# Kernel tuning notes

Measured on AMD Instinct MI355X. Metric: run time of the kernel, lower is better.

Reference implementation:

```python
import jax, jax.numpy as jnp
import numpy as np

EMBED_DIM = 2048
HEAD_DIM = 128
BLOCK = 2048
BATCH = 8


def setup_inputs() -> dict:
    key = jax.random.key(0)
    kx, kq, kk, kv = jax.random.split(key, 4)
    x = jax.random.normal(kx, (BATCH, BLOCK, EMBED_DIM), dtype=jnp.float32)
    # torch nn.Linear(embed_dim, head_dim, bias=False) weight shape: [head_dim, embed_dim]
    s = 1.0 / np.sqrt(EMBED_DIM)
    Wq = jax.random.uniform(kq, (HEAD_DIM, EMBED_DIM), jnp.float32, -s, s)
    Wk = jax.random.uniform(kk, (HEAD_DIM, EMBED_DIM), jnp.float32, -s, s)
    Wv = jax.random.uniform(kv, (HEAD_DIM, EMBED_DIM), jnp.float32, -s, s)
    return {"x": x, "Wq": Wq, "Wk": Wk, "Wv": Wv}


def reference(x, Wq, Wk, Wv):
    B, T, C = x.shape
    # projections: y = x @ W.T
    q = jnp.einsum('btc,hc->bth', x, Wq)   # [B,T,H]
    k = jnp.einsum('btc,hc->bth', x, Wk)
    v = jnp.einsum('btc,hc->bth', x, Wv)
    # NOTE: original scales by embed_dim**0.5, not head_dim**0.5
    scale = 1.0 / jnp.sqrt(jnp.float32(C))
    logits = jnp.einsum('bth,bsh->bts', q, k) * scale  # [B,T,T]
    # causal mask (is_decoder=True)
    causal = jnp.tril(jnp.ones((T, T), dtype=bool))
    logits = jnp.where(causal, logits, -jnp.inf)
    weights = jax.nn.softmax(logits, axis=-1)
    attention = jnp.einsum('bts,bsh->bth', weights, v)  # [B,T,H]
    return attention
```

## Files before the change

### kernel.cpp

```cpp
#include <hip/hip_runtime.h>
#include <hip/hip_bf16.h>
#include <stdint.h>

constexpr int B    = 8;
constexpr int T    = 2048;
constexpr int EMB  = 2048;
constexpr int HD   = 128;
constexpr int M    = B * T;
constexpr int NW   = 3 * HD;

typedef __attribute__((ext_vector_type(8))) short short8;
typedef __attribute__((ext_vector_type(4))) float f32x4;

__device__ inline unsigned short f2bf(float f) {
    union { float f; unsigned int u; } v; v.f = f;
    unsigned int x = v.u;
    unsigned int r = (x + 0x7FFFu + ((x >> 16) & 1u)) >> 16;
    return (unsigned short)r;
}

__device__ inline unsigned int cvt_pk_bf16(float a, float b) {
    unsigned int r;
    asm volatile("v_cvt_pk_bf16_f32 %0, %1, %2" : "=v"(r) : "v"(a), "v"(b));
    return r;
}

__global__ __launch_bounds__(256) void conv_w(
    const float* __restrict__ Wq, const float* __restrict__ Wk, const float* __restrict__ Wv,
    unsigned short* __restrict__ Wb)
{
    int base = (blockIdx.x * 256 + threadIdx.x) * 8;
    int row = base >> 11, col = base & 2047;
    const float* src;
    if (row < 128)      src = Wq + (size_t)row * EMB + col;
    else if (row < 256) src = Wk + (size_t)(row - 128) * EMB + col;
    else                src = Wv + (size_t)(row - 256) * EMB + col;
    float4 a = *(const float4*)src;
    float4 b = *(const float4*)(src + 4);
    short8 sv;
    sv[0] = f2bf(a.x); sv[1] = f2bf(a.y); sv[2] = f2bf(a.z); sv[3] = f2bf(a.w);
    sv[4] = f2bf(b.x); sv[5] = f2bf(b.y); sv[6] = f2bf(b.z); sv[7] = f2bf(b.w);
    *(short8*)(Wb + base) = sv;
}

constexpr int PBM = 32;
constexpr int PBK = 64;
constexpr int PNT = EMB / PBK;

__global__ __launch_bounds__(256) void qkv_proj(
    const float* __restrict__ x, const unsigned short* __restrict__ Wb,
    unsigned short* __restrict__ Qb, unsigned short* __restrict__ Kb,
    unsigned short* __restrict__ VtG)
{
    __shared__ unsigned short Asm[2][PBM * PBK];
    __shared__ unsigned short Bsm[NW * PBK];

    const int m0   = blockIdx.x * PBM;
    const int tid  = threadIdx.x;
    const int lane = tid & 63;
    const int w    = tid >> 6;
    const int lo   = lane & 15;
    const int hi   = lane >> 4;

    const int ar = tid >> 3;
    const int as = tid & 7;
    const float* asrc = x + (size_t)(m0 + ar) * EMB + as * 8;

    f32x4 acc[2][6];
#pragma unroll
    for (int i = 0; i < 2; ++i)
#pragma unroll
        for (int j = 0; j < 6; ++j) acc[i][j] = (f32x4)0.0f;

    float4 a0, a1;
    auto issueA = [&](int k0) {
        a0 = *(const float4*)(asrc + k0);
        a1 = *(const float4*)(asrc + k0 + 4);
    };
    auto writeA = [&](int buf) {
        uint4 p;
        p.x = cvt_pk_bf16(a0.x, a0.y);
        p.y = cvt_pk_bf16(a0.z, a0.w);
        p.z = cvt_pk_bf16(a1.x, a1.y);
        p.w = cvt_pk_bf16(a1.z, a1.w);
        int ps = as ^ (ar & 7);
        *(uint4*)&Asm[buf][ar * PBK + ps * 8] = p;
    };
    auto stageB = [&](int k0) {
#pragma unroll
        for (int it = 0; it < 12; ++it) {
            int c = it * 256 + tid;
            int row = c >> 3;
            int lseg = (c & 7) ^ (row & 7);
            __builtin_amdgcn_global_load_lds(
                (const __attribute__((address_space(1))) unsigned int*)
                    (Wb + (size_t)row * EMB + k0 + lseg * 8),
                (__attribute__((address_space(3))) unsigned int*)
                    ((char*)&Bsm[0] + (it * 256 + w * 64) * 16),
                16, 0, 0);
        }
    };
    auto compute = [&](int buf) {
#pragma unroll
        for (int kk = 0; kk < 2; ++kk) {
            short8 af[2], bf[6];
#pragma unroll
            for (int i = 0; i < 2; ++i) {
                int R = i * 16 + lo;
                int pseg = (kk * 4 + hi) ^ (R & 7);
                af[i] = *(const short8*)&Asm[buf][R * PBK + pseg * 8];
            }
#pragma unroll
            for (int j = 0; j < 6; ++j) {
                int n = w * 96 + j * 16 + lo;
                int pseg = (kk * 4 + hi) ^ (n & 7);
                bf[j] = *(const short8*)&Bsm[n * PBK + pseg * 8];
            }
#pragma unroll
            for (int i = 0; i < 2; ++i)
#pragma unroll
                for (int j = 0; j < 6; ++j)
                    acc[i][j] = __builtin_amdgcn_mfma_f32_16x16x32_bf16(af[i], bf[j], acc[i][j], 0, 0, 0);
        }
    };

    issueA(0);
    stageB(0);
    writeA(0);
    asm volatile("s_waitcnt vmcnt(0) lgkmcnt(0)" ::: "memory");
    __builtin_amdgcn_s_barrier();

    int cur = 0;
    for (int t = 0; t < PNT; ++t) {
        if (t + 1 < PNT) issueA((t + 1) * PBK);
        compute(cur);
        __builtin_amdgcn_s_barrier();
        if (t + 1 < PNT) {
            stageB((t + 1) * PBK);
            writeA(cur ^ 1);
            asm volatile("s_waitcnt vmcnt(0) lgkmcnt(0)" ::: "memory");
            __builtin_amdgcn_s_barrier();
        }
        cur ^= 1;
    }

    const int b = m0 >> 11;
#pragma unroll
    for (int i = 0; i < 2; ++i) {
        int mrow0 = m0 + i * 16 + hi * 4;
#pragma unroll
        for (int j = 0; j < 6; ++j) {
            int cw = w * 6 + j;
            int colbase = cw * 16 + lo;
            if (cw < 8) {
#pragma unroll
                for (int r = 0; r < 4; ++r)
                    Qb[(size_t)(mrow0 + r) * HD + colbase] = f2bf(acc[i][j][r]);
            } else if (cw < 16) {
#pragma unroll
                for (int r = 0; r < 4; ++r)
                    Kb[(size_t)(mrow0 + r) * HD + (colbase - 128)] = f2bf(acc[i][j][r]);
            } else {
                int h = colbase - 256;
                int tloc = mrow0 - b * T;
                ushort4 pv;
                pv.x = f2bf(acc[i][j][0]); pv.y = f2bf(acc[i][j][1]);
                pv.z = f2bf(acc[i][j][2]); pv.w = f2bf(acc[i][j][3]);
                *(ushort4*)(VtG + ((size_t)(b * HD + h)) * T + tloc) = pv;
            }
        }
    }
}

constexpr int QB = 64;
constexpr int KB = 64;
constexpr int STILES = 8;

__global__ __launch_bounds__(256) void attn_fwd(
    const unsigned short* __restrict__ Qb,
    const unsigned short* __restrict__ Kb,
    const unsigned short* __restrict__ VtG,
    float* __restrict__ out,
    float* __restrict__ part_o, float* __restrict__ part_ml,
    int use_split)
{
    const int b  = blockIdx.y;
    int bx = blockIdx.x;
    int qt, s, nsplit;
    if (use_split) {
        if (bx < 8)       { qt = bx;               s = 0; }
        else if (bx < 24) { qt = 8  + (bx - 8) / 2;  s = (bx - 8) & 1; }
        else if (bx < 48) { qt = 16 + (bx - 24) / 3; s = (bx - 24) % 3; }
        else              { qt = 24 + (bx - 48) / 4; s = (bx - 48) & 3; }
        nsplit = qt / 8 + 1;
    } else {
        qt = bx; s = 0; nsplit = 1;
    }
    const int q0 = qt * QB;
    int t0 = s * STILES;
    int t1 = t0 + STILES; if (t1 > qt + 1) t1 = qt + 1;

    const int tid  = threadIdx.x;
    const int lane = tid & 63;
    const int w    = tid >> 6;
    const int lo   = lane & 15;
    const int hi   = lane >> 4;

    __shared__ unsigned short Ks[KB][HD + 8];
    __shared__ unsigned short Vt[HD][KB + 16];
    __shared__ unsigned short Ps[QB][KB + 8];

    short8 qf[4];
    {
        int row = q0 + w * 16 + lo;
        const unsigned short* qp = Qb + ((size_t)b * T + row) * HD + hi * 8;
#pragma unroll
        for (int ks = 0; ks < 4; ++ks) qf[ks] = *(const short8*)(qp + ks * 32);
    }

    float mrow[4], lrow[4];
    f32x4 o[8];
#pragma unroll
    for (int r = 0; r < 4; ++r) { mrow[r] = -1e30f; lrow[r] = 0.0f; }
#pragma unroll
    for (int n = 0; n < 8; ++n) o[n] = (f32x4)0.0f;

    const float scale2 = 0.022097086912079608f * 1.4426950408889634f;
    const int qrow_base = q0 + w * 16 + hi * 4;

    for (int t = t0; t < t1; ++t) {
        const int kv0 = t * KB;
#pragma unroll
        for (int it = 0; it < 4; ++it) {
            int c = tid + it * 256;
            int row = c >> 4, c8 = (c & 15) * 8;
            *(short8*)&Ks[row][c8] =
                *(const short8*)(Kb + ((size_t)b * T + kv0 + row) * HD + c8);
        }
#pragma unroll
        for (int it = 0; it < 4; ++it) {
            int c = tid + it * 256;
            int row = c >> 3, c8 = (c & 7) * 8;
            *(short8*)&Vt[row][c8] =
                *(const short8*)(VtG + (size_t)(b * HD + row) * T + kv0 + c8);
        }
        __syncthreads();

        f32x4 sa[4];
#pragma unroll
        for (int j = 0; j < 4; ++j) sa[j] = (f32x4)0.0f;
#pragma unroll
        for (int ks = 0; ks < 4; ++ks) {
#pragma unroll
            for (int j = 0; j < 4; ++j) {
                short8 bf = *(const short8*)&Ks[j * 16 + lo][ks * 32 + hi * 8];
                sa[j] = __builtin_amdgcn_mfma_f32_16x16x32_bf16(qf[ks], bf, sa[j], 0, 0, 0);
            }
        }

        const bool diag = (t == qt);
        float alpha[4];
#pragma unroll
        for (int r = 0; r < 4; ++r) {
            const int qrow = qrow_base + r;
            float rm = -1e30f;
#pragma unroll
            for (int j = 0; j < 4; ++j) {
                float v = sa[j][r] * scale2;
                if (diag) {
                    int kv = kv0 + j * 16 + lo;
                    v = (kv <= qrow) ? v : -1e30f;
                }
                sa[j][r] = v;
                rm = fmaxf(rm, v);
            }
            rm = fmaxf(rm, __shfl_xor(rm, 1));
            rm = fmaxf(rm, __shfl_xor(rm, 2));
            rm = fmaxf(rm, __shfl_xor(rm, 4));
            rm = fmaxf(rm, __shfl_xor(rm, 8));
            float mn = fmaxf(mrow[r], rm);
            alpha[r] = exp2f(mrow[r] - mn);
            mrow[r] = mn;
            float ls = 0.0f;
#pragma unroll
            for (int j = 0; j < 4; ++j) {
                float p = exp2f(sa[j][r] - mn);
                sa[j][r] = p;
                ls += p;
            }
            ls += __shfl_xor(ls, 1);
            ls += __shfl_xor(ls, 2);
            ls += __shfl_xor(ls, 4);
            ls += __shfl_xor(ls, 8);
            lrow[r] = lrow[r] * alpha[r] + ls;
        }
#pragma unroll
        for (int n = 0; n < 8; ++n)
#pragma unroll
            for (int r = 0; r < 4; ++r) o[n][r] *= alpha[r];

#pragma unroll
        for (int r = 0; r < 4; ++r)
#pragma unroll
            for (int j = 0; j < 4; ++j)
                Ps[w * 16 + hi * 4 + r][j * 16 + lo] = f2bf(sa[j][r]);
        __syncthreads();

#pragma unroll
        for (int ks = 0; ks < 2; ++ks) {
            short8 af = *(const short8*)&Ps[w * 16 + lo][ks * 32 + hi * 8];
#pragma unroll
            for (int n = 0; n < 8; ++n) {
                short8 bv = *(const short8*)&Vt[n * 16 + lo][ks * 32 + hi * 8];
                o[n] = __builtin_amdgcn_mfma_f32_16x16x32_bf16(af, bv, o[n], 0, 0, 0);
            }
        }
        __syncthreads();
    }

    if (nsplit == 1) {
#pragma unroll
        for (int n = 0; n < 8; ++n) {
            int h = n * 16 + lo;
#pragma unroll
            for (int r = 0; r < 4; ++r) {
                int row = qrow_base + r;
                out[((size_t)b * T + row) * HD + h] = o[n][r] / lrow[r];
            }
        }
    } else {
        const size_t slot = (size_t)(b * 32 + qt) * 4 + s;
        float* po = part_o + slot * (QB * HD);
#pragma unroll
        for (int n = 0; n < 8; ++n) {
            int h = n * 16 + lo;
#pragma unroll
            for (int r = 0; r < 4; ++r)
                po[(w * 16 + hi * 4 + r) * HD + h] = o[n][r];
        }
        if (lo == 0) {
            float* pm = part_ml + slot * (QB * 2);
#pragma unroll
            for (int r = 0; r < 4; ++r) {
                pm[(w * 16 + hi * 4 + r) * 2 + 0] = mrow[r];
                pm[(w * 16 + hi * 4 + r) * 2 + 1] = lrow[r];
            }
        }
    }
}

__global__ __launch_bounds__(256) void attn_combine(
    const float* __restrict__ part_o, const float* __restrict__ part_ml,
    float* __restrict__ out)
{
    const int qt = 8 + blockIdx.x;
    const int b  = blockIdx.y;
    const int ns = qt / 8 + 1;
    const int tid = threadIdx.x;
    const int row = tid >> 2;
    const int c0  = (tid & 3) * 32;
    const size_t slot0 = (size_t)(b * 32 + qt) * 4;

    float mi[4], li[4];
    float m = -1e30f;
#pragma unroll 4
    for (int i = 0; i < ns; ++i) {
        mi[i] = part_ml[(slot0 + i) * (QB * 2) + row * 2 + 0];
        li[i] = part_ml[(slot0 + i) * (QB * 2) + row * 2 + 1];
        m = fmaxf(m, mi[i]);
    }
    float L = 0.0f, f[4];
#pragma unroll 4
    for (int i = 0; i < ns; ++i) {
        f[i] = exp2f(mi[i] - m);
        L += li[i] * f[i];
    }
    const float inv = 1.0f / L;

    float4 acc[8];
#pragma unroll
    for (int k = 0; k < 8; ++k) acc[k] = make_float4(0.f, 0.f, 0.f, 0.f);
#pragma unroll 4
    for (int i = 0; i < ns; ++i) {
        const float4* src = (const float4*)(part_o + (slot0 + i) * (QB * HD) + row * HD + c0);
#pragma unroll
        for (int k = 0; k < 8; ++k) {
            float4 v = src[k];
            acc[k].x += f[i] * v.x; acc[k].y += f[i] * v.y;
            acc[k].z += f[i] * v.z; acc[k].w += f[i] * v.w;
        }
    }
    float4* dst = (float4*)(out + ((size_t)b * T + qt * QB + row) * HD + c0);
#pragma unroll
    for (int k = 0; k < 8; ++k) {
        float4 v = acc[k];
        dst[k] = make_float4(v.x * inv, v.y * inv, v.z * inv, v.w * inv);
    }
}

extern "C" void kernel_launch(void* const* d_in, const int* in_sizes, int n_in,
                              void* d_out, int out_size, void* d_ws, size_t ws_size,
                              hipStream_t stream)
{
    const float* x  = (const float*)d_in[0];
    const float* Wq = (const float*)d_in[1];
    const float* Wk = (const float*)d_in[2];
    const float* Wv = (const float*)d_in[3];
    float* out = (float*)d_out;

    const size_t off_Wb = 0;
    const size_t off_Q  = off_Wb + (size_t)NW * EMB * 2;
    const size_t off_K  = off_Q  + (size_t)M * HD * 2;
    const size_t off_V  = off_K  + (size_t)M * HD * 2;
    const size_t off_po = off_V  + (size_t)M * HD * 2;
    const size_t off_ml = off_po + (size_t)1024 * QB * HD * 4;
    const size_t total  = off_ml + (size_t)1024 * QB * 2 * 4;

    char* ws = (char*)d_ws;
    unsigned short* Wb  = (unsigned short*)(ws + off_Wb);
    unsigned short* Qb  = (unsigned short*)(ws + off_Q);
    unsigned short* Kb  = (unsigned short*)(ws + off_K);
    unsigned short* VtG = (unsigned short*)(ws + off_V);
    float* part_o  = (float*)(ws + off_po);
    float* part_ml = (float*)(ws + off_ml);

    const int use_split = (ws_size >= total) ? 1 : 0;

    conv_w<<<dim3((NW * EMB) / (256 * 8)), 256, 0, stream>>>(Wq, Wk, Wv, Wb);
    qkv_proj<<<dim3(M / PBM), 256, 0, stream>>>(x, Wb, Qb, Kb, VtG);
    attn_fwd<<<dim3(use_split ? 80 : 32, B), 256, 0, stream>>>(
        Qb, Kb, VtG, out, part_o, part_ml, use_split);
    if (use_split)
        attn_combine<<<dim3(24, B), 256, 0, stream>>>(part_o, part_ml, out);
}
```

Measured before the change: 113.3 us.

## Enlarge QKV projection tile to 64 rows with 8 waves and double-buffered weights

The QKV projection block grows from 32 to 64 rows of x and from 256 to 512 threads, arranged as 2x4 waves. Each weight tile loaded into shared memory is therefore reused across twice as many rows, which halves weight traffic per output. The weight tile is also double-buffered and prefetched before the compute step, which drops one barrier per k-step and overlaps the weight load with the MFMA work. In exchange, shared memory per block rises to about 112KB, so only one block fits per CU, and the grid shrinks to 256 blocks, which lowers occupancy and latency hiding.

```diff
diff --git a/kernel.cpp b/kernel.cpp
--- a/kernel.cpp
+++ b/kernel.cpp
@@ -43,22 +43,24 @@
     *(short8*)(Wb + base) = sv;
 }
 
-constexpr int PBM = 32;
+constexpr int PBM = 64;
 constexpr int PBK = 64;
 constexpr int PNT = EMB / PBK;
 
-__global__ __launch_bounds__(256) void qkv_proj(
+__global__ __launch_bounds__(512) void qkv_proj(
     const float* __restrict__ x, const unsigned short* __restrict__ Wb,
     unsigned short* __restrict__ Qb, unsigned short* __restrict__ Kb,
     unsigned short* __restrict__ VtG)
 {
     __shared__ unsigned short Asm[2][PBM * PBK];
-    __shared__ unsigned short Bsm[NW * PBK];
+    __shared__ unsigned short Bsm[2][NW * PBK];
 
     const int m0   = blockIdx.x * PBM;
     const int tid  = threadIdx.x;
     const int lane = tid & 63;
     const int w    = tid >> 6;
+    const int wr   = w >> 2;
+    const int wc   = w & 3;
     const int lo   = lane & 15;
     const int hi   = lane >> 4;
 
@@ -86,17 +88,17 @@
         int ps = as ^ (ar & 7);
         *(uint4*)&Asm[buf][ar * PBK + ps * 8] = p;
     };
-    auto stageB = [&](int k0) {
-#pragma unroll
-        for (int it = 0; it < 12; ++it) {
-            int c = it * 256 + tid;
+    auto stageB = [&](int k0, int buf) {
+#pragma unroll
+        for (int it = 0; it < 6; ++it) {
+            int c = it * 512 + tid;
             int row = c >> 3;
             int lseg = (c & 7) ^ (row & 7);
             __builtin_amdgcn_global_load_lds(
                 (const __attribute__((address_space(1))) unsigned int*)
                     (Wb + (size_t)row * EMB + k0 + lseg * 8),
                 (__attribute__((address_space(3))) unsigned int*)
-                    ((char*)&Bsm[0] + (it * 256 + w * 64) * 16),
+                    ((char*)&Bsm[buf][0] + (it * 512 + w * 64) * 16),
                 16, 0, 0);
         }
     };
@@ -106,15 +108,15 @@
             short8 af[2], bf[6];
 #pragma unroll
             for (int i = 0; i < 2; ++i) {
-                int R = i * 16 + lo;
+                int R = wr * 32 + i * 16 + lo;
                 int pseg = (kk * 4 + hi) ^ (R & 7);
                 af[i] = *(const short8*)&Asm[buf][R * PBK + pseg * 8];
             }
 #pragma unroll
             for (int j = 0; j < 6; ++j) {
-                int n = w * 96 + j * 16 + lo;
+                int n = wc * 96 + j * 16 + lo;
                 int pseg = (kk * 4 + hi) ^ (n & 7);
-                bf[j] = *(const short8*)&Bsm[n * PBK + pseg * 8];
+                bf[j] = *(const short8*)&Bsm[buf][n * PBK + pseg * 8];
             }
 #pragma unroll
             for (int i = 0; i < 2; ++i)
@@ -125,32 +127,32 @@
     };
 
     issueA(0);
-    stageB(0);
+    stageB(0, 0);
     writeA(0);
     asm volatile("s_waitcnt vmcnt(0) lgkmcnt(0)" ::: "memory");
     __builtin_amdgcn_s_barrier();
 
-    int cur = 0;
     for (int t = 0; t < PNT; ++t) {
-        if (t + 1 < PNT) issueA((t + 1) * PBK);
-        compute(cur);
-        __builtin_amdgcn_s_barrier();
+        const int buf = t & 1;
         if (t + 1 < PNT) {
-            stageB((t + 1) * PBK);
-            writeA(cur ^ 1);
+            issueA((t + 1) * PBK);
+            stageB((t + 1) * PBK, buf ^ 1);
+        }
+        compute(buf);
+        if (t + 1 < PNT) {
+            writeA(buf ^ 1);
             asm volatile("s_waitcnt vmcnt(0) lgkmcnt(0)" ::: "memory");
             __builtin_amdgcn_s_barrier();
         }
-        cur ^= 1;
     }
 
     const int b = m0 >> 11;
 #pragma unroll
     for (int i = 0; i < 2; ++i) {
-        int mrow0 = m0 + i * 16 + hi * 4;
+        int mrow0 = m0 + wr * 32 + i * 16 + hi * 4;
 #pragma unroll
         for (int j = 0; j < 6; ++j) {
-            int cw = w * 6 + j;
+            int cw = wc * 6 + j;
             int colbase = cw * 16 + lo;
             if (cw < 8) {
 #pragma unroll
@@ -427,7 +429,7 @@
     const int use_split = (ws_size >= total) ? 1 : 0;
 
     conv_w<<<dim3((NW * EMB) / (256 * 8)), 256, 0, stream>>>(Wq, Wk, Wv, Wb);
-    qkv_proj<<<dim3(M / PBM), 256, 0, stream>>>(x, Wb, Qb, Kb, VtG);
+    qkv_proj<<<dim3(M / PBM), 512, 0, stream>>>(x, Wb, Qb, Kb, VtG);
     attn_fwd<<<dim3(use_split ? 80 : 32, B), 256, 0, stream>>>(
         Qb, Kb, VtG, out, part_o, part_ml, use_split);
     if (use_split)
```

After: 115.4 us. Within noise of the previous version (+1.8%).
